# Kernel optimization log

Hardware: AMD Instinct MI355X
Metric: run time of the kernel (lower is better)

Reference implementation:

```python
import jax, jax.numpy as jnp
import numpy as np

BATCH, T, C = 32, 600, 64
DEPTH = 2            # logsig depth 2 -> [increments, Levy areas]
N_SEGMENTS = 50
N_HIDDENS = 512
LOGSIG_CH = C + C * (C - 1) // 2   # 2080, Lyndon-word count at depth 2
IN_SIZE = C + LOGSIG_CH            # 2144 = logsig + start point


def _t_vec(nT, n_segments):
    # matches: [int(round(x)) for x in np.linspace(1, nT, n_segments+1)]
    return np.asarray([int(round(v)) for v in np.linspace(1, nT, n_segments + 1)])


def setup_inputs() -> dict:
    key = jax.random.key(0)
    k0, k1, k2, k3, k4 = jax.random.split(key, 5)
    x = jax.random.normal(k0, (BATCH, T, C), jnp.float32)
    s = 1.0 / np.sqrt(N_HIDDENS)
    w_ih = jax.random.uniform(k1, (4 * N_HIDDENS, IN_SIZE), jnp.float32, -s, s)
    w_hh = jax.random.uniform(k2, (4 * N_HIDDENS, N_HIDDENS), jnp.float32, -s, s)
    b_ih = jax.random.uniform(k3, (4 * N_HIDDENS,), jnp.float32, -s, s)
    b_hh = jax.random.uniform(k4, (4 * N_HIDDENS,), jnp.float32, -s, s)
    return {"x": x, "w_ih": w_ih, "w_hh": w_hh, "b_ih": b_ih, "b_hh": b_hh}


def _logsig_and_start(x):
    """Depth-2 segmented log-signature + segment start points.
    Returns (logsig (B,S,LOGSIG_CH), start (B,S,C))."""
    B, nT, c = x.shape
    tv = _t_vec(nT, N_SEGMENTS)
    starts = tv[:-1] - 1               # segment start frame indices
    ends = tv[1:] - 1                  # segment end frame indices
    # step s (between frames s and s+1) belongs to segment i iff tv[i]-1 <= s < tv[i+1]-1
    step_ids = jnp.asarray(np.searchsorted(tv[1:] - 1, np.arange(nT - 1), side='right'))
    dx = x[:, 1:] - x[:, :-1]                            # (B, T-1, C)
    # per-step outer product x_{t-} (X) dx_t, then segmented sum over steps
    prod = jnp.einsum('btc,btd->btcd', x[:, :-1], dx)    # (B, T-1, C, C)
    Q = jax.ops.segment_sum(jnp.moveaxis(prod, 1, 0), step_ids,
                            num_segments=N_SEGMENTS)      # (S, B, C, C)
    xa = x[:, starts]                                    # (B, S, C)
    xb = x[:, ends]
    inc = xb - xa                                        # level-1 logsig
    # shift origin to segment start: P = sum (X_rel (X) dX)
    P = jnp.moveaxis(Q, 0, 1) - jnp.einsum('bsc,bsd->bscd', xa, inc)
    A = 0.5 * (P - jnp.swapaxes(P, -1, -2))              # Levy area (antisym)
    iu, ju = np.triu_indices(c, 1)                       # Lyndon words (i,j), i<j, lex order
    logsig = jnp.concatenate([inc, A[:, :, iu, ju]], axis=-1)
    return logsig, xa


def _lstm(feats, w_ih, w_hh, b_ih, b_hh):
    B = feats.shape[0]
    H = N_HIDDENS
    gx = jnp.einsum('bsf,gf->bsg', feats, w_ih) + b_ih + b_hh  # (B,S,4H)

    def step(carry, g_t):
        h, cc = carry
        g = g_t + h @ w_hh.T
        i, f, gg, o = jnp.split(g, 4, axis=-1)
        i = jax.nn.sigmoid(i); f = jax.nn.sigmoid(f)
        gg = jnp.tanh(gg); o = jax.nn.sigmoid(o)
        cc = f * cc + i * gg
        h = o * jnp.tanh(cc)
        return (h, cc), h

    h0 = jnp.zeros((B, H), feats.dtype)
    (_, _), hs = jax.lax.scan(step, (h0, h0), jnp.moveaxis(gx, 1, 0))
    return jnp.moveaxis(hs, 0, 1)                        # (B, S, H)


def reference(x, w_ih, w_hh, b_ih, b_hh):
    logsig, x_sp = _logsig_and_start(x)
    feats = jnp.concatenate([logsig, x_sp], axis=-1)      # (B, S, IN_SIZE)
    return _lstm(feats, w_ih, w_hh, b_ih, b_hh)
```

## Files before the change

kernel.cpp:

```cpp
#include <hip/hip_runtime.h>
#include <hip/hip_cooperative_groups.h>
#include <math.h>

namespace cg = cooperative_groups;

typedef _Float16 f16;
typedef _Float16 f16x8 __attribute__((ext_vector_type(8)));
typedef _Float16 f16x4 __attribute__((ext_vector_type(4)));
typedef float    f32x4 __attribute__((ext_vector_type(4)));

#define BATCH 32
#define TT    600
#define CC    64
#define SEG   50
#define HH    512
#define G4    2048
#define FF    2144
#define MM    1600
#define MP    1664
#define NPAIR 2016
#define CVB   512

struct TV { int v[51]; };

__device__ __forceinline__ void async_copy16(char* lds, const char* g) {
  __builtin_amdgcn_global_load_lds(
      (const __attribute__((address_space(1))) unsigned int*)g,
      (__attribute__((address_space(3))) unsigned int*)lds, 16, 0, 0);
}

__device__ __forceinline__ float sigm(float x) { return 1.f / (1.f + __expf(-x)); }
__device__ __forceinline__ float tanh_(float x) {
  float ax = fabsf(x);
  float e  = __expf(2.f * ax);
  float t  = 1.f - 2.f / (e + 1.f);
  return x < 0.f ? -t : t;
}
__device__ __forceinline__ unsigned short f16_bits(f16 v) {
  union { f16 f; unsigned short u; } c; c.f = v; return c.u;
}

__global__ void prep_kernel(const float* __restrict__ x, f16* __restrict__ fhi, TV tv,
                            const float4* __restrict__ w_ih, const float4* __restrict__ w_hh,
                            f16x4* __restrict__ w16, f16x4* __restrict__ whh16,
                            unsigned int* __restrict__ ready) {
  __shared__ float xs[13 * CC];
  int m   = blockIdx.x;
  int tid = threadIdx.x;

  if (m >= MP) {
    int cb   = m - MP;
    int gtid = cb * 256 + tid;
    int nth  = CVB * 256;
    for (int i = gtid; i < G4 * FF / 4; i += nth) {
      float4 v = w_ih[i];
      f16x4 o = {(f16)v.x, (f16)v.y, (f16)v.z, (f16)v.w};
      w16[i] = o;
    }
    for (int i = gtid; i < G4 * HH / 4; i += nth) {
      float4 v = w_hh[i];
      f16x4 o = {(f16)v.x, (f16)v.y, (f16)v.z, (f16)v.w};
      whh16[i] = o;
    }
    if (cb == 0)
      for (int i = tid; i < 512; i += 256) ready[i] = 0u;
    return;
  }

  f16* rhi = fhi + (size_t)m * FF;
  if (m >= MM) {
    unsigned int* a = (unsigned int*)rhi;
    for (int i = tid; i < FF / 2; i += 256) a[i] = 0u;
    return;
  }
  int bb = m & 31, ss = m >> 5;
  int t0 = tv.v[ss] - 1, t1 = tv.v[ss + 1] - 1;
  int len = t1 - t0;
  for (int i = tid; i < (len + 1) * CC; i += 256)
    xs[i] = x[(size_t)bb * TT * CC + (size_t)(t0 + (i >> 6)) * CC + (i & 63)];
  __syncthreads();

  if (tid < CC) {
    float xa  = xs[tid];
    float inc = xs[len * CC + tid] - xa;
    rhi[tid] = (f16)inc;
    rhi[2080 + tid] = (f16)xa;
  }

  int p0 = tid * 8;
  if (p0 < NPAIR) {
    int c = 0, rem = p0;
    while (rem >= 63 - c) { rem -= 63 - c; c++; }
    int d = c + 1 + rem;
    int cs[8], dd[8];
#pragma unroll
    for (int i = 0; i < 8; i++) {
      cs[i] = c; dd[i] = d;
      d++; if (d == 64) { c++; d = c + 1; }
    }
    float acc[8], xc[8], xd[8];
#pragma unroll
    for (int i = 0; i < 8; i++) { acc[i] = 0.f; xc[i] = xs[cs[i]]; xd[i] = xs[dd[i]]; }
    for (int t = 1; t <= len; t++) {
#pragma unroll
      for (int i = 0; i < 8; i++) {
        float nc = xs[t * CC + cs[i]], nd = xs[t * CC + dd[i]];
        acc[i] += xc[i] * (nd - xd[i]) - xd[i] * (nc - xc[i]);
        xc[i] = nc; xd[i] = nd;
      }
    }
#pragma unroll
    for (int i = 0; i < 8; i++) {
      int ci = cs[i], di = dd[i];
      float xac = xs[ci], xad = xs[di];
      float incc = xs[len * CC + ci] - xac, incd = xs[len * CC + di] - xad;
      float v = 0.5f * acc[i] - 0.5f * (xac * incd - xad * incc);
      rhi[64 + p0 + i] = (f16)v;
    }
  }
}

__global__ __launch_bounds__(256) void gemm_kernel(
    const f16* __restrict__ fhi, const f16* __restrict__ w16,
    const float* __restrict__ bih, const float* __restrict__ bhh,
    float* __restrict__ gx) {
  __shared__ f16 smem[6 * 1024];
  int tid  = threadIdx.x;
  int lane = tid & 63;
  int wn   = tid >> 6;

  int id = blockIdx.x;
  int x8 = id & 7;
  int j  = id >> 3;
  int mt = j % 26;
  int nt = (x8 << 1) | (j / 26);
  int m0 = mt * 64;
  int n0 = nt * 128;

  char* ldsA = (char*)&smem[0];
  char* ldsB = (char*)&smem[2048];

  int rowq = tid >> 2;
  int colq = (tid & 3) * 8;
  const f16* pa  = fhi + (size_t)(m0 + rowq) * FF + colq;
  const f16* pb0 = w16 + (size_t)(n0 + rowq) * FF + colq;
  const f16* pb1 = pb0 + (size_t)64 * FF;
  int ldst = tid * 16;

  f32x4 zero4 = {0.f, 0.f, 0.f, 0.f};
  f32x4 acc[4][2];
#pragma unroll
  for (int i = 0; i < 4; i++) { acc[i][0] = zero4; acc[i][1] = zero4; }

  int quad16 = (lane >> 4) * 16;
  int am = lane & 15;

  for (int kt = 0; kt < FF / 32; kt++) {
    int koff = kt * 32;
    async_copy16(ldsA + ldst,        (const char*)(pa + koff));
    async_copy16(ldsB + ldst,        (const char*)(pb0 + koff));
    async_copy16(ldsB + 4096 + ldst, (const char*)(pb1 + koff));
    __syncthreads();

    f16x8 bfr[2];
#pragma unroll
    for (int ni = 0; ni < 2; ni++)
      bfr[ni] = *(const f16x8*)(ldsB + (wn * 32 + ni * 16 + am) * 64 + quad16);
#pragma unroll
    for (int mi = 0; mi < 4; mi++) {
      f16x8 ah = *(const f16x8*)(ldsA + (mi * 16 + am) * 64 + quad16);
#pragma unroll
      for (int ni = 0; ni < 2; ni++)
        acc[mi][ni] = __builtin_amdgcn_mfma_f32_16x16x32_f16(ah, bfr[ni], acc[mi][ni], 0, 0, 0);
    }
    __syncthreads();
  }

#pragma unroll
  for (int ni = 0; ni < 2; ni++) {
    int ncol = n0 + wn * 32 + ni * 16 + (lane & 15);
    float bv = bih[ncol] + bhh[ncol];
#pragma unroll
    for (int mi = 0; mi < 4; mi++) {
      int mrow = m0 + mi * 16 + (lane >> 4) * 4;
#pragma unroll
      for (int r = 0; r < 4; r++)
        gx[(size_t)(mrow + r) * G4 + ncol] = acc[mi][ni][r] + bv;
    }
  }
}

__global__ __launch_bounds__(256, 1) void lstm_kernel(
    const float* __restrict__ gx, const f16* __restrict__ whh16,
    unsigned short* __restrict__ hbuf, unsigned int* __restrict__ ready,
    float* __restrict__ out) {
  __shared__ f16 hs[BATCH * HH];
  __shared__ float gbuf[4][BATCH][16];

  int tid  = threadIdx.x;
  int lane = tid & 63;
  int gate = tid >> 6;
  int u0   = blockIdx.x * 16;
  int wg   = blockIdx.x;

  f16x8 bf[16];
  {
    const f16* wrow = whh16 + (size_t)(gate * HH + u0 + (lane & 15)) * HH + (lane >> 4) * 8;
#pragma unroll
    for (int ks = 0; ks < 16; ks++) bf[ks] = *(const f16x8*)(wrow + ks * 32);
  }

  int b1 = tid >> 4;
  int ul = tid & 15;
  float cst0 = 0.f, cst1 = 0.f;
  int aq  = (lane >> 4);
  int am  = (lane & 15);
  int col = lane & 15;
  int rbase = (lane >> 4) * 4;

  for (int s = 0; s < SEG; s++) {
    float gxr0[4], gxr1[4];
#pragma unroll
    for (int r = 0; r < 4; r++) {
      int b = rbase + r;
      gxr0[r] = gx[(size_t)((s << 5) + b) * G4 + gate * HH + u0 + col];
      gxr1[r] = gx[(size_t)((s << 5) + b + 16) * G4 + gate * HH + u0 + col];
    }

    f32x4 acc0 = {0.f, 0.f, 0.f, 0.f};
    f32x4 acc1 = {0.f, 0.f, 0.f, 0.f};

    if (s > 0) {
      unsigned int tgt = (unsigned int)s;
      if (tid < 32) {
        while (__hip_atomic_load(&ready[tid * 16], __ATOMIC_RELAXED,
                                 __HIP_MEMORY_SCOPE_AGENT) < tgt)
          __builtin_amdgcn_s_sleep(1);
      }
      __syncthreads();

      const unsigned long long* hrd =
          (const unsigned long long*)(hbuf + (size_t)(s & 1) * (BATCH * HH));
      unsigned long long v[16];
#pragma unroll
      for (int i = 0; i < 16; i++)
        v[i] = __hip_atomic_load(hrd + i * 256 + tid, __ATOMIC_RELAXED,
                                 __HIP_MEMORY_SCOPE_AGENT);
      unsigned long long* hw = (unsigned long long*)hs;
#pragma unroll
      for (int i = 0; i < 16; i++) hw[i * 256 + tid] = v[i];
      __syncthreads();

#pragma unroll
      for (int ks = 0; ks < 16; ks++) {
        f16x8 a0 = *(const f16x8*)((char*)hs + (((ks * 4 + aq) * 32) + am) * 16);
        f16x8 a1 = *(const f16x8*)((char*)hs + (((ks * 4 + aq) * 32) + 16 + am) * 16);
        acc0 = __builtin_amdgcn_mfma_f32_16x16x32_f16(a0, bf[ks], acc0, 0, 0, 0);
        acc1 = __builtin_amdgcn_mfma_f32_16x16x32_f16(a1, bf[ks], acc1, 0, 0, 0);
      }
    }

#pragma unroll
    for (int r = 0; r < 4; r++) {
      int b = rbase + r;
      gbuf[gate][b][col]      = acc0[r] + gxr0[r];
      gbuf[gate][b + 16][col] = acc1[r] + gxr1[r];
    }
    __syncthreads();

    unsigned short* hwr = hbuf + (size_t)((s + 1) & 1) * (BATCH * HH);
    int k = u0 + ul;
    float h0, h1;
    {
      float i_ = sigm(gbuf[0][b1][ul]), f_ = sigm(gbuf[1][b1][ul]);
      float g_ = tanh_(gbuf[2][b1][ul]), o_ = sigm(gbuf[3][b1][ul]);
      cst0 = f_ * cst0 + i_ * g_;
      h0 = o_ * tanh_(cst0);
      out[(size_t)(b1 * SEG + s) * HH + k] = h0;
    }
    {
      int b2 = b1 + 16;
      float i_ = sigm(gbuf[0][b2][ul]), f_ = sigm(gbuf[1][b2][ul]);
      float g_ = tanh_(gbuf[2][b2][ul]), o_ = sigm(gbuf[3][b2][ul]);
      cst1 = f_ * cst1 + i_ * g_;
      h1 = o_ * tanh_(cst1);
      out[(size_t)(b2 * SEG + s) * HH + k] = h1;
    }

    if (s < SEG - 1) {
      __hip_atomic_store(hwr + ((k >> 3) * 32 + b1) * 8 + (k & 7),
                         f16_bits((f16)h0), __ATOMIC_RELAXED, __HIP_MEMORY_SCOPE_AGENT);
      __hip_atomic_store(hwr + ((k >> 3) * 32 + (b1 + 16)) * 8 + (k & 7),
                         f16_bits((f16)h1), __ATOMIC_RELAXED, __HIP_MEMORY_SCOPE_AGENT);
      __syncthreads();
      if (tid == 0)
        __hip_atomic_store(&ready[wg * 16], (unsigned int)(s + 1),
                           __ATOMIC_RELAXED, __HIP_MEMORY_SCOPE_AGENT);
    }
  }
}

extern "C" void kernel_launch(void* const* d_in, const int* in_sizes, int n_in,
                              void* d_out, int out_size, void* d_ws, size_t ws_size,
                              hipStream_t stream) {
  const float* x    = (const float*)d_in[0];
  const float* w_ih = (const float*)d_in[1];
  const float* w_hh = (const float*)d_in[2];
  const float* b_ih = (const float*)d_in[3];
  const float* b_hh = (const float*)d_in[4];
  float* out = (float*)d_out;

  char* ws = (char*)d_ws;
  f16*   fhi   = (f16*)(ws + 0);
  f16*   w16   = (f16*)(ws + 7135232);
  f16*   whh16 = (f16*)(ws + 15921152);
  float* gx    = (float*)(ws + 18018304);
  unsigned short* hbuf  = (unsigned short*)(ws + 31649792);
  unsigned int*   ready = (unsigned int*)(ws + 31715328);

  TV tv;
  double step = 599.0 / 50.0;
  for (int i = 0; i <= 50; i++) {
    double v = (double)i * step + 1.0;
    tv.v[i] = (int)nearbyint(v);
  }
  tv.v[50] = 600;

  prep_kernel<<<dim3(MP + CVB), dim3(256), 0, stream>>>(
      x, fhi, tv, (const float4*)w_ih, (const float4*)w_hh,
      (f16x4*)w16, (f16x4*)whh16, ready);
  gemm_kernel<<<dim3(416), dim3(256), 0, stream>>>(fhi, w16, b_ih, b_hh, gx);

  void* args[] = { (void*)&gx, (void*)&whh16, (void*)&hbuf, (void*)&ready, (void*)&out };
  hipLaunchCooperativeKernel((void*)lstm_kernel, dim3(32), dim3(256), args, 0, stream);
}
```

Measured before the change: 298.7 us.

## Fuse input GEMM with LSTM recurrence so recurrence overlaps GEMM tiles

Merges the input-projection GEMM and the LSTM recurrence into one cooperative kernel. 32 blocks run the recurrence and 208 worker blocks compute GEMM tiles ordered by M-tile, i.e. by segment. Each worker publishes a per-M-tile completion counter with atomic stores, and the recurrence blocks wait on the counter before reading that segment's gate inputs. The aim is to start the serial recurrence before the whole GEMM finishes and to drop a kernel launch. In exchange it adds atomic loads and stores on gx, spin-waits, and larger LDS use, and it depends on all 240 blocks being co-resident.

```diff
diff --git a/kernel.cpp b/kernel.cpp
--- a/kernel.cpp
+++ b/kernel.cpp
@@ -20,6 +20,7 @@
 #define MP    1664
 #define NPAIR 2016
 #define CVB   512
+#define WRK   208
 
 struct TV { int v[51]; };
 
@@ -38,6 +39,12 @@
 }
 __device__ __forceinline__ unsigned short f16_bits(f16 v) {
   union { f16 f; unsigned short u; } c; c.f = v; return c.u;
+}
+__device__ __forceinline__ unsigned int f32_bits(float v) {
+  union { float f; unsigned int u; } c; c.f = v; return c.u;
+}
+__device__ __forceinline__ float bits_f32(unsigned int v) {
+  union { unsigned int u; float f; } c; c.u = v; return c.f;
 }
 
 __global__ void prep_kernel(const float* __restrict__ x, f16* __restrict__ fhi, TV tv,
@@ -63,7 +70,7 @@
       whh16[i] = o;
     }
     if (cb == 0)
-      for (int i = tid; i < 512; i += 256) ready[i] = 0u;
+      for (int i = tid; i < 544; i += 256) ready[i] = 0u;
     return;
   }
 
@@ -120,85 +127,88 @@
   }
 }
 
-__global__ __launch_bounds__(256) void gemm_kernel(
+__global__ __launch_bounds__(256) void fused_kernel(
     const f16* __restrict__ fhi, const f16* __restrict__ w16,
     const float* __restrict__ bih, const float* __restrict__ bhh,
-    float* __restrict__ gx) {
-  __shared__ f16 smem[6 * 1024];
+    const f16* __restrict__ whh16, float* __restrict__ gx,
+    unsigned short* __restrict__ hbuf, unsigned int* __restrict__ ready,
+    unsigned int* __restrict__ gxcnt, float* __restrict__ out) {
+  __shared__ __align__(16) char smem[40960];
   int tid  = threadIdx.x;
   int lane = tid & 63;
-  int wn   = tid >> 6;
-
-  int id = blockIdx.x;
-  int x8 = id & 7;
-  int j  = id >> 3;
-  int mt = j % 26;
-  int nt = (x8 << 1) | (j / 26);
-  int m0 = mt * 64;
-  int n0 = nt * 128;
-
-  char* ldsA = (char*)&smem[0];
-  char* ldsB = (char*)&smem[2048];
-
-  int rowq = tid >> 2;
-  int colq = (tid & 3) * 8;
-  const f16* pa  = fhi + (size_t)(m0 + rowq) * FF + colq;
-  const f16* pb0 = w16 + (size_t)(n0 + rowq) * FF + colq;
-  const f16* pb1 = pb0 + (size_t)64 * FF;
-  int ldst = tid * 16;
-
-  f32x4 zero4 = {0.f, 0.f, 0.f, 0.f};
-  f32x4 acc[4][2];
-#pragma unroll
-  for (int i = 0; i < 4; i++) { acc[i][0] = zero4; acc[i][1] = zero4; }
-
-  int quad16 = (lane >> 4) * 16;
-  int am = lane & 15;
-
-  for (int kt = 0; kt < FF / 32; kt++) {
-    int koff = kt * 32;
-    async_copy16(ldsA + ldst,        (const char*)(pa + koff));
-    async_copy16(ldsB + ldst,        (const char*)(pb0 + koff));
-    async_copy16(ldsB + 4096 + ldst, (const char*)(pb1 + koff));
-    __syncthreads();
-
-    f16x8 bfr[2];
-#pragma unroll
-    for (int ni = 0; ni < 2; ni++)
-      bfr[ni] = *(const f16x8*)(ldsB + (wn * 32 + ni * 16 + am) * 64 + quad16);
-#pragma unroll
-    for (int mi = 0; mi < 4; mi++) {
-      f16x8 ah = *(const f16x8*)(ldsA + (mi * 16 + am) * 64 + quad16);
-#pragma unroll
-      for (int ni = 0; ni < 2; ni++)
-        acc[mi][ni] = __builtin_amdgcn_mfma_f32_16x16x32_f16(ah, bfr[ni], acc[mi][ni], 0, 0, 0);
-    }
-    __syncthreads();
-  }
-
-#pragma unroll
-  for (int ni = 0; ni < 2; ni++) {
-    int ncol = n0 + wn * 32 + ni * 16 + (lane & 15);
-    float bv = bih[ncol] + bhh[ncol];
-#pragma unroll
-    for (int mi = 0; mi < 4; mi++) {
-      int mrow = m0 + mi * 16 + (lane >> 4) * 4;
-#pragma unroll
-      for (int r = 0; r < 4; r++)
-        gx[(size_t)(mrow + r) * G4 + ncol] = acc[mi][ni][r] + bv;
-    }
-  }
-}
-
-__global__ __launch_bounds__(256, 1) void lstm_kernel(
-    const float* __restrict__ gx, const f16* __restrict__ whh16,
-    unsigned short* __restrict__ hbuf, unsigned int* __restrict__ ready,
-    float* __restrict__ out) {
-  __shared__ f16 hs[BATCH * HH];
-  __shared__ float gbuf[4][BATCH][16];
-
-  int tid  = threadIdx.x;
-  int lane = tid & 63;
+
+  if (blockIdx.x >= 32) {
+    int w  = blockIdx.x - 32;
+    int wn = tid >> 6;
+    char* ldsA = smem;
+    char* ldsB = smem + 4096;
+    int rowq = tid >> 2;
+    int colq = (tid & 3) * 8;
+    int ldst = tid * 16;
+    int quad16 = (lane >> 4) * 16;
+    int am = lane & 15;
+    unsigned int* gxa = (unsigned int*)gx;
+
+    for (int t = 0; t < 2; t++) {
+      int id = w + t * WRK;
+      int mt = id >> 4, nt = id & 15;
+      int m0 = mt * 64, n0 = nt * 128;
+
+      const f16* pa  = fhi + (size_t)(m0 + rowq) * FF + colq;
+      const f16* pb0 = w16 + (size_t)(n0 + rowq) * FF + colq;
+      const f16* pb1 = pb0 + (size_t)64 * FF;
+
+      f32x4 zero4 = {0.f, 0.f, 0.f, 0.f};
+      f32x4 acc[4][2];
+#pragma unroll
+      for (int i = 0; i < 4; i++) { acc[i][0] = zero4; acc[i][1] = zero4; }
+
+      for (int kt = 0; kt < FF / 32; kt++) {
+        int koff = kt * 32;
+        async_copy16(ldsA + ldst,        (const char*)(pa + koff));
+        async_copy16(ldsB + ldst,        (const char*)(pb0 + koff));
+        async_copy16(ldsB + 4096 + ldst, (const char*)(pb1 + koff));
+        __syncthreads();
+
+        f16x8 bfr[2];
+#pragma unroll
+        for (int ni = 0; ni < 2; ni++)
+          bfr[ni] = *(const f16x8*)(ldsB + (wn * 32 + ni * 16 + am) * 64 + quad16);
+#pragma unroll
+        for (int mi = 0; mi < 4; mi++) {
+          f16x8 ah = *(const f16x8*)(ldsA + (mi * 16 + am) * 64 + quad16);
+#pragma unroll
+          for (int ni = 0; ni < 2; ni++)
+            acc[mi][ni] = __builtin_amdgcn_mfma_f32_16x16x32_f16(ah, bfr[ni], acc[mi][ni], 0, 0, 0);
+        }
+        __syncthreads();
+      }
+
+#pragma unroll
+      for (int ni = 0; ni < 2; ni++) {
+        int ncol = n0 + wn * 32 + ni * 16 + (lane & 15);
+        float bv = bih[ncol] + bhh[ncol];
+#pragma unroll
+        for (int mi = 0; mi < 4; mi++) {
+          int mrow = m0 + mi * 16 + (lane >> 4) * 4;
+#pragma unroll
+          for (int r = 0; r < 4; r++)
+            __hip_atomic_store(gxa + (size_t)(mrow + r) * G4 + ncol,
+                               f32_bits(acc[mi][ni][r] + bv),
+                               __ATOMIC_RELAXED, __HIP_MEMORY_SCOPE_AGENT);
+        }
+      }
+      __syncthreads();
+      if (tid == 0)
+        __hip_atomic_fetch_add(&gxcnt[mt], 1u, __ATOMIC_RELAXED,
+                               __HIP_MEMORY_SCOPE_AGENT);
+    }
+    return;
+  }
+
+  f16* hs = (f16*)smem;
+  float* gb = (float*)(smem + 32768);
+
   int gate = tid >> 6;
   int u0   = blockIdx.x * 16;
   int wg   = blockIdx.x;
@@ -217,14 +227,28 @@
   int am  = (lane & 15);
   int col = lane & 15;
   int rbase = (lane >> 4) * 4;
+  const unsigned int* gxa = (const unsigned int*)gx;
 
   for (int s = 0; s < SEG; s++) {
+    if ((s & 1) == 0) {
+      if (tid == 0) {
+        while (__hip_atomic_load(&gxcnt[s >> 1], __ATOMIC_RELAXED,
+                                 __HIP_MEMORY_SCOPE_AGENT) < 16u)
+          __builtin_amdgcn_s_sleep(1);
+      }
+      __syncthreads();
+    }
+
     float gxr0[4], gxr1[4];
 #pragma unroll
     for (int r = 0; r < 4; r++) {
       int b = rbase + r;
-      gxr0[r] = gx[(size_t)((s << 5) + b) * G4 + gate * HH + u0 + col];
-      gxr1[r] = gx[(size_t)((s << 5) + b + 16) * G4 + gate * HH + u0 + col];
+      gxr0[r] = bits_f32(__hip_atomic_load(
+          gxa + (size_t)((s << 5) + b) * G4 + gate * HH + u0 + col,
+          __ATOMIC_RELAXED, __HIP_MEMORY_SCOPE_AGENT));
+      gxr1[r] = bits_f32(__hip_atomic_load(
+          gxa + (size_t)((s << 5) + b + 16) * G4 + gate * HH + u0 + col,
+          __ATOMIC_RELAXED, __HIP_MEMORY_SCOPE_AGENT));
     }
 
     f32x4 acc0 = {0.f, 0.f, 0.f, 0.f};
@@ -263,8 +287,8 @@
 #pragma unroll
     for (int r = 0; r < 4; r++) {
       int b = rbase + r;
-      gbuf[gate][b][col]      = acc0[r] + gxr0[r];
-      gbuf[gate][b + 16][col] = acc1[r] + gxr1[r];
+      gb[(gate * 32 + b) * 16 + col]      = acc0[r] + gxr0[r];
+      gb[(gate * 32 + b + 16) * 16 + col] = acc1[r] + gxr1[r];
     }
     __syncthreads();
 
@@ -272,16 +296,16 @@
     int k = u0 + ul;
     float h0, h1;
     {
-      float i_ = sigm(gbuf[0][b1][ul]), f_ = sigm(gbuf[1][b1][ul]);
-      float g_ = tanh_(gbuf[2][b1][ul]), o_ = sigm(gbuf[3][b1][ul]);
+      float i_ = sigm(gb[(0 * 32 + b1) * 16 + ul]), f_ = sigm(gb[(1 * 32 + b1) * 16 + ul]);
+      float g_ = tanh_(gb[(2 * 32 + b1) * 16 + ul]), o_ = sigm(gb[(3 * 32 + b1) * 16 + ul]);
       cst0 = f_ * cst0 + i_ * g_;
       h0 = o_ * tanh_(cst0);
       out[(size_t)(b1 * SEG + s) * HH + k] = h0;
     }
     {
       int b2 = b1 + 16;
-      float i_ = sigm(gbuf[0][b2][ul]), f_ = sigm(gbuf[1][b2][ul]);
-      float g_ = tanh_(gbuf[2][b2][ul]), o_ = sigm(gbuf[3][b2][ul]);
+      float i_ = sigm(gb[(0 * 32 + b2) * 16 + ul]), f_ = sigm(gb[(1 * 32 + b2) * 16 + ul]);
+      float g_ = tanh_(gb[(2 * 32 + b2) * 16 + ul]), o_ = sigm(gb[(3 * 32 + b2) * 16 + ul]);
       cst1 = f_ * cst1 + i_ * g_;
       h1 = o_ * tanh_(cst1);
       out[(size_t)(b2 * SEG + s) * HH + k] = h1;
@@ -317,6 +341,7 @@
   float* gx    = (float*)(ws + 18018304);
   unsigned short* hbuf  = (unsigned short*)(ws + 31649792);
   unsigned int*   ready = (unsigned int*)(ws + 31715328);
+  unsigned int*   gxcnt = ready + 512;
 
   TV tv;
   double step = 599.0 / 50.0;
@@ -329,8 +354,9 @@
   prep_kernel<<<dim3(MP + CVB), dim3(256), 0, stream>>>(
       x, fhi, tv, (const float4*)w_ih, (const float4*)w_hh,
       (f16x4*)w16, (f16x4*)whh16, ready);
-  gemm_kernel<<<dim3(416), dim3(256), 0, stream>>>(fhi, w16, b_ih, b_hh, gx);
-
-  void* args[] = { (void*)&gx, (void*)&whh16, (void*)&hbuf, (void*)&ready, (void*)&out };
-  hipLaunchCooperativeKernel((void*)lstm_kernel, dim3(32), dim3(256), args, 0, stream);
-}
+
+  void* args[] = { (void*)&fhi, (void*)&w16, (void*)&b_ih, (void*)&b_hh,
+                   (void*)&whh16, (void*)&gx, (void*)&hbuf, (void*)&ready,
+                   (void*)&gxcnt, (void*)&out };
+  hipLaunchCooperativeKernel((void*)fused_kernel, dim3(32 + WRK), dim3(256), args, 0, stream);
+}
```

After: 301.4 us. About the same (+0.9%).
